# Optimization experiments

Hardware: AMD Instinct MI355X
Metric: run time of the kernel (lower is better)

The kernel has to match this reference:

```python
import jax, jax.numpy as jnp
import numpy as np

DT = 0.01   # integrator timestep (init kwarg dt)
N = 2048    # connectome.n
T = 2048    # number of timesteps
MAG_SCALE = 1e-06  # magnitude_scaling_factor applied at init


def setup_inputs() -> dict:
    key = jax.random.key(0)
    ks = jax.random.split(key, 8)
    inp = jax.random.normal(ks[0], (T, N), dtype=jnp.float32)
    sparsity_c = (jax.random.uniform(ks[1], (N, N)) < 0.1).astype(jnp.float32)
    se = (jax.random.uniform(ks[2], (N, N)) < 0.05).astype(jnp.float32)
    sparsity_e = jnp.maximum(se, se.T)
    signs_c = jnp.sign(jax.random.normal(ks[3], (N, N))).astype(jnp.float32)
    magnitudes_c = MAG_SCALE * jax.random.uniform(ks[4], (N, N), dtype=jnp.float32)
    magnitudes_e = MAG_SCALE * jax.random.uniform(ks[5], (N, N), dtype=jnp.float32)
    bias = jax.random.uniform(ks[6], (N,), dtype=jnp.float32, minval=0.01, maxval=0.02)
    tau = jax.random.uniform(ks[7], (N,), dtype=jnp.float32, minval=DT, maxval=0.2)
    hidden_init = jnp.zeros((N,), dtype=jnp.float32)
    return {
        'input': inp,
        'sparsity_c': sparsity_c,
        'sparsity_e': sparsity_e,
        'signs_c': signs_c,
        'magnitudes_c': magnitudes_c,
        'magnitudes_e': magnitudes_e,
        'bias': bias,
        'tau': tau,
        'hidden_init': hidden_init,
    }


def reference(input, sparsity_c, sparsity_e, signs_c, magnitudes_c, magnitudes_e, bias, tau, hidden_init):
    # clamp magnitudes at 0 (torch does in-place clamp_ on .data; inputs are
    # nonnegative so this is an identity with matching gradients)
    mc = jnp.maximum(magnitudes_c, 0.0)
    me = jnp.maximum(magnitudes_e, 0.0)
    W_c = sparsity_c * mc * signs_c                 # [N, N] chemical weights
    W_e = sparsity_e * (me + me.T)                  # [N, N] symmetric gap junctions
    we_row = jnp.sum(W_e, axis=1)                   # [N] row sums for diffusion term
    tau_c = jnp.maximum(tau, DT)
    alpha = DT / tau_c                              # [N]

    def step(x, u_t):
        # x: [N] hidden state, u_t: [N] external input at time t
        chem = W_c @ jax.nn.relu(x)                 # sparse chemical input
        # elec[i] = sum_j W_e[i,j] * (x[j] - x[i])  (gap-junction diffusion)
        elec = W_e @ x - we_row * x
        rec = chem + elec
        x_new = alpha * (rec + bias + u_t - x) + x
        return x_new, (x_new, rec)

    _, (hidden_states, recurrent_in) = jax.lax.scan(step, hidden_init, input)
    external_in = input  # cat of input[t].unsqueeze(0) over t == input itself
    return hidden_states, recurrent_in, external_in
```

## Files before the change

kernel.cpp:

```cpp
#include <hip/hip_runtime.h>
#include <hip/hip_bf16.h>

typedef unsigned short u16;
typedef __attribute__((ext_vector_type(8))) short bf16x8;
typedef __attribute__((ext_vector_type(4))) float f32x4;

#define N_ 2048
#define T_ 2048
#define K_ 4096
#define DT_ 0.01f
#define C_ 64
#define L_ 32

#define AS1 __attribute__((address_space(1)))
#define AS3 __attribute__((address_space(3)))
#define GLDS(gp, lp) __builtin_amdgcn_global_load_lds((const AS1 void*)(gp), (AS3 void*)(lp), 16, 0, 0)

__device__ __forceinline__ float waveReduceSum(float v){
#pragma unroll
  for (int o = 32; o > 0; o >>= 1) v += __shfl_down(v, o, 64);
  return v;
}

__global__ __launch_bounds__(256) void k1_build_zero_scan1A(
    const float* __restrict__ sc, const float* __restrict__ mc, const float* __restrict__ sg,
    __hip_bfloat16* __restrict__ Bt, float* __restrict__ we_row,
    const float* __restrict__ u, const float* __restrict__ bias, const float* __restrict__ tau,
    float* __restrict__ S1){
  int b = blockIdx.x, t = threadIdx.x;
  if (b < 2048){
    size_t g = ((size_t)b * 256 + t) * 8;
    float4 s0 = *(const float4*)(sc + g), s1 = *(const float4*)(sc + g + 4);
    float4 m0 = *(const float4*)(mc + g), m1 = *(const float4*)(mc + g + 4);
    float4 g0 = *(const float4*)(sg + g), g1 = *(const float4*)(sg + g + 4);
    __align__(16) __hip_bfloat16 o[8];
    o[0] = __float2bfloat16(s0.x * fmaxf(m0.x, 0.f) * g0.x);
    o[1] = __float2bfloat16(s0.y * fmaxf(m0.y, 0.f) * g0.y);
    o[2] = __float2bfloat16(s0.z * fmaxf(m0.z, 0.f) * g0.z);
    o[3] = __float2bfloat16(s0.w * fmaxf(m0.w, 0.f) * g0.w);
    o[4] = __float2bfloat16(s1.x * fmaxf(m1.x, 0.f) * g1.x);
    o[5] = __float2bfloat16(s1.y * fmaxf(m1.y, 0.f) * g1.y);
    o[6] = __float2bfloat16(s1.z * fmaxf(m1.z, 0.f) * g1.z);
    o[7] = __float2bfloat16(s1.w * fmaxf(m1.w, 0.f) * g1.w);
    int n = (int)(g >> 11);
    int kk = (int)(g & 2047);
    *(uint4*)&Bt[(size_t)n * K_ + kk] = *(const uint4*)o;
  } else if (b < 2056){
    we_row[(b - 2048) * 256 + t] = 0.f;
  } else {
    int bb = b - 2056;
    int c = bb >> 3;
    int i = (bb & 7) * 256 + t;
    float a  = DT_ / fmaxf(tau[i], DT_);
    float m  = 1.f - a;
    float bv = bias[i];
    float s  = 0.f;
    const float* up = u + (size_t)(c * L_) * N_ + i;
#pragma unroll 8
    for (int j = 0; j < L_; ++j)
      s = __builtin_fmaf(m, s, a * (bv + up[(size_t)j * N_]));
    S1[(size_t)c * N_ + i] = s;
  }
}

__global__ __launch_bounds__(256) void k2_prep_scan1B(
    const float* __restrict__ se, const float* __restrict__ me,
    __hip_bfloat16* __restrict__ Bt, float* __restrict__ we_row,
    const float* __restrict__ tau, const float* __restrict__ h0,
    const float* __restrict__ S1, float* __restrict__ X1){
  __shared__ float L0[64 * 65];
  __shared__ float L1[64 * 65];
  int b = blockIdx.x, t = threadIdx.x;
  if (b < 528){
    int lane = t & 63, w = t >> 6;
    int bi = 0, off = 0;
    while (off + (32 - bi) <= b){ off += 32 - bi; ++bi; }
    int bj = bi + (b - off);
    int n0 = bi * 64, j0 = bj * 64;
#pragma unroll
    for (int k = 0; k < 16; ++k){
      int r = w + 4 * k;
      size_t i1 = (size_t)(n0 + r) * N_ + j0 + lane;
      L0[r * 65 + lane] = se[i1] * fmaxf(me[i1], 0.f);
      size_t i2 = (size_t)(j0 + r) * N_ + n0 + lane;
      L1[lane * 65 + r] = se[i2] * fmaxf(me[i2], 0.f);
    }
    __syncthreads();
#pragma unroll
    for (int k = 0; k < 16; ++k){
      int nr = w + 4 * k;
      float v = L0[nr * 65 + lane] + L1[nr * 65 + lane];
      Bt[(size_t)(n0 + nr) * K_ + N_ + j0 + lane] = __float2bfloat16(v);
      L0[nr * 65 + lane] = v;
      float s = waveReduceSum(v);
      if (lane == 0) atomicAdd(&we_row[n0 + nr], s);
    }
    if (bi != bj){
      __syncthreads();
#pragma unroll
      for (int k = 0; k < 16; ++k){
        int jr = w + 4 * k;
        float v = L0[lane * 65 + jr];
        Bt[(size_t)(j0 + jr) * K_ + N_ + n0 + lane] = __float2bfloat16(v);
        float s = waveReduceSum(v);
        if (lane == 0) atomicAdd(&we_row[j0 + jr], s);
      }
    }
  } else {
    int i = (b - 528) * 256 + t;
    float a = DT_ / fmaxf(tau[i], DT_);
    float m = 1.f - a;
    float mL = m * m; mL = mL * mL; mL = mL * mL; mL = mL * mL; mL = mL * mL;
    float x = h0[i];
#pragma unroll 16
    for (int c = 0; c < C_; ++c){
      X1[(size_t)c * N_ + i] = x;
      x = __builtin_fmaf(mL, x, S1[(size_t)c * N_ + i]);
    }
  }
}

__global__ __launch_bounds__(256) void scan1C(const float* __restrict__ u, const float* __restrict__ bias,
                                              const float* __restrict__ tau, const float* __restrict__ X,
                                              __hip_bfloat16* __restrict__ A){
  int b = blockIdx.x;
  int c = b >> 3;
  int i = (b & 7) * 256 + threadIdx.x;
  float a  = DT_ / fmaxf(tau[i], DT_);
  float m  = 1.f - a;
  float bb = bias[i];
  float x  = X[(size_t)c * N_ + i];
  int t0 = c * L_;
#pragma unroll 8
  for (int j = 0; j < L_; ++j){
    size_t t = (size_t)(t0 + j);
    A[t * K_ + i]      = __float2bfloat16(fmaxf(x, 0.f));
    A[t * K_ + N_ + i] = __float2bfloat16(x);
    x = __builtin_fmaf(m, x, a * (bb + u[t * N_ + i]));
  }
}

__global__ __launch_bounds__(256) void scan2A(const float* __restrict__ u, const float* __restrict__ rec,
                                              const float* __restrict__ bias, const float* __restrict__ tau,
                                              const float* __restrict__ we_row, float* __restrict__ S){
  int b = blockIdx.x;
  int c = b >> 3;
  int i = (b & 7) * 256 + threadIdx.x;
  float a  = DT_ / fmaxf(tau[i], DT_);
  float wr = we_row[i];
  float m  = 1.f - a - a * wr;
  float bb = bias[i];
  float s  = 0.f;
  size_t base = (size_t)(c * L_) * N_ + i;
#pragma unroll 8
  for (int j = 0; j < L_; ++j){
    size_t o = base + (size_t)j * N_;
    s = __builtin_fmaf(m, s, a * (rec[o] + bb + u[o]));
  }
  S[(size_t)c * N_ + i] = s;
}

__global__ __launch_bounds__(256) void scan2B(const float* __restrict__ tau, const float* __restrict__ h0,
                                              const float* __restrict__ we_row, const float* __restrict__ S,
                                              float* __restrict__ X){
  int i = blockIdx.x * 256 + threadIdx.x;
  float a  = DT_ / fmaxf(tau[i], DT_);
  float wr = we_row[i];
  float m  = 1.f - a - a * wr;
  float mL = m * m; mL = mL * mL; mL = mL * mL; mL = mL * mL; mL = mL * mL;
  float x = h0[i];
#pragma unroll 16
  for (int c = 0; c < C_; ++c){
    X[(size_t)c * N_ + i] = x;
    x = __builtin_fmaf(mL, x, S[(size_t)c * N_ + i]);
  }
}

__global__ __launch_bounds__(256) void scan2C(const float* __restrict__ u, const float* __restrict__ bias,
                                              const float* __restrict__ tau, const float* __restrict__ we_row,
                                              const float* __restrict__ X,
                                              float* __restrict__ rec, float* __restrict__ hidden,
                                              float* __restrict__ ext){
  int b = blockIdx.x;
  int c = b >> 3;
  int i = (b & 7) * 256 + threadIdx.x;
  float a  = DT_ / fmaxf(tau[i], DT_);
  float wr = we_row[i];
  float m  = 1.f - a - a * wr;
  float bb = bias[i];
  float x  = X[(size_t)c * N_ + i];
  int t0 = c * L_;
#pragma unroll 4
  for (int j = 0; j < L_; ++j){
    size_t o = (size_t)(t0 + j) * N_ + i;
    float g  = rec[o];
    float uu = u[o];
    float cc = a * (g + bb + uu);
    rec[o]   = g - wr * x;
    if (ext) ext[o] = uu;
    x = __builtin_fmaf(m, x, cc);
    hidden[o] = x;
  }
}

__global__ __launch_bounds__(256) void copy_ext(const float4* __restrict__ in, float4* __restrict__ out){
  int i = blockIdx.x * 256 + threadIdx.x;
  out[i] = in[i];
}

__global__ __launch_bounds__(512, 4) void gemm_bt(const u16* __restrict__ A, const u16* __restrict__ B,
                                                  float* __restrict__ C){
  __shared__ __align__(16) u16 As[3][128 * 64];
  __shared__ __align__(16) u16 Bs[3][64 * 64];
  int bid = blockIdx.x;
  int j8 = bid >> 3;
  int bm = ((bid & 7) * 2 + (j8 >> 5)) * 128;
  int bn = (j8 & 31) * 64;
  int t = threadIdx.x;
  int lane = t & 63;
  int wv = t >> 6;
  int wr = (wv >> 1) * 32;
  int wc = (wv & 1) * 32;

  int srow = t >> 3;
  int scol = ((t & 7) ^ (srow & 7)) * 8;
  const u16* Ap = A + (size_t)(bm + srow) * K_ + scol;
  const u16* Bp = B + (size_t)(bn + srow) * K_ + scol;
  int lb = wv * 512;

  const f32x4 z = {0.f, 0.f, 0.f, 0.f};
  f32x4 acc[2][2];
#pragma unroll
  for (int mi = 0; mi < 2; ++mi)
#pragma unroll
    for (int ni = 0; ni < 2; ++ni) acc[mi][ni] = z;

  auto stage = [&](int buf, int kt){
    int k0 = kt * 64;
    GLDS(Ap + k0, &As[buf][lb]);
    GLDS(Ap + (size_t)64 * K_ + k0, &As[buf][4096 + lb]);
    GLDS(Bp + k0, &Bs[buf][lb]);
  };

  int fr = lane & 15, q = lane >> 4;
  auto compute = [&](int cur){
#pragma unroll
    for (int ks = 0; ks < 2; ++ks){
      bf16x8 af[2], bv[2];
#pragma unroll
      for (int mi = 0; mi < 2; ++mi){
        int r = wr + mi * 16 + fr;
        af[mi] = *(const bf16x8*)&As[cur][r * 64 + ((((ks << 2) + q) ^ (r & 7)) << 3)];
      }
#pragma unroll
      for (int ni = 0; ni < 2; ++ni){
        int r = wc + ni * 16 + fr;
        bv[ni] = *(const bf16x8*)&Bs[cur][r * 64 + ((((ks << 2) + q) ^ (r & 7)) << 3)];
      }
      __builtin_amdgcn_s_setprio(1);
#pragma unroll
      for (int mi = 0; mi < 2; ++mi)
#pragma unroll
        for (int ni = 0; ni < 2; ++ni)
          acc[mi][ni] = __builtin_amdgcn_mfma_f32_16x16x32_bf16(af[mi], bv[ni], acc[mi][ni], 0, 0, 0);
      __builtin_amdgcn_s_setprio(0);
    }
  };

  stage(0, 0);
  stage(1, 1);
  int cb = 0, sb = 2;
  for (int tt = 0; tt < 62; ++tt){
    stage(sb, tt + 2);
    asm volatile("s_waitcnt vmcnt(6)\n\ts_barrier" ::: "memory");
    compute(cb);
    asm volatile("s_barrier" ::: "memory");
    cb = (cb == 2) ? 0 : cb + 1;
    sb = (sb == 2) ? 0 : sb + 1;
  }
  asm volatile("s_waitcnt vmcnt(3)\n\ts_barrier" ::: "memory");
  compute(cb);
  cb = (cb == 2) ? 0 : cb + 1;
  asm volatile("s_waitcnt vmcnt(0)\n\ts_barrier" ::: "memory");
  compute(cb);

#pragma unroll
  for (int mi = 0; mi < 2; ++mi){
#pragma unroll
    for (int ni = 0; ni < 2; ++ni){
      int col = bn + wc + ni * 16 + fr;
#pragma unroll
      for (int r = 0; r < 4; ++r){
        int row = bm + wr + mi * 16 + q * 4 + r;
        C[(size_t)row * N_ + col] = acc[mi][ni][r];
      }
    }
  }
}

extern "C" void kernel_launch(void* const* d_in, const int* in_sizes, int n_in,
                              void* d_out, int out_size, void* d_ws, size_t ws_size,
                              hipStream_t stream){
  const float* input = (const float*)d_in[0];
  const float* sp_c  = (const float*)d_in[1];
  const float* sp_e  = (const float*)d_in[2];
  const float* sg_c  = (const float*)d_in[3];
  const float* mg_c  = (const float*)d_in[4];
  const float* mg_e  = (const float*)d_in[5];
  const float* bias  = (const float*)d_in[6];
  const float* tau   = (const float*)d_in[7];
  const float* h0    = (const float*)d_in[8];

  float* hidden = (float*)d_out;
  float* rec    = hidden + (size_t)T_ * N_;
  float* ext    = rec    + (size_t)T_ * N_;
  __hip_bfloat16* Abuf = (__hip_bfloat16*)hidden;
  __hip_bfloat16* Bt   = (__hip_bfloat16*)ext;
  float* S1 = rec;
  float* X1 = rec + (size_t)N_ * C_;
  float* we_row = (float*)d_ws;

  bool ws_ok = ws_size >= (size_t)(2048 + 2 * C_ * N_) * 4;
  float* S2 = ws_ok ? (we_row + 2048) : ext;
  float* X2 = S2 + (size_t)C_ * N_;

  k1_build_zero_scan1A<<<2568, 256, 0, stream>>>(sp_c, mg_c, sg_c, Bt, we_row,
                                                 input, bias, tau, S1);
  k2_prep_scan1B<<<536, 256, 0, stream>>>(sp_e, mg_e, Bt, we_row, tau, h0, S1, X1);
  scan1C<<<8 * C_, 256, 0, stream>>>(input, bias, tau, X1, Abuf);

  gemm_bt<<<512, 512, 0, stream>>>((const u16*)Abuf, (const u16*)Bt, rec);

  scan2A<<<8 * C_, 256, 0, stream>>>(input, rec, bias, tau, we_row, S2);
  scan2B<<<8, 256, 0, stream>>>(tau, h0, we_row, S2, X2);
  scan2C<<<8 * C_, 256, 0, stream>>>(input, bias, tau, we_row, X2, rec, hidden,
                                     ws_ok ? ext : nullptr);
  if (!ws_ok)
    copy_ext<<<T_ * N_ / 1024, 256, 0, stream>>>((const float4*)input, (float4*)ext);
}
```

Baseline: 130.8 us.

## Enlarge GEMM tiles to 128x128 and split K in two with atomic accumulation

Rewrites the bf16 GEMM to use 128x128 output tiles with 256 threads, each wave computing a 64x64 sub-tile. Shared memory drops from triple to double buffering. K is split in half across blocks, and partial results are combined with atomicAdd into a buffer zeroed by a new memset. The intent is more data reuse per block and more MFMA work per wave. In exchange it adds a full-output memset and atomic read-modify-write traffic, and shortens the prefetch depth.

```diff
diff --git a/kernel.cpp b/kernel.cpp
--- a/kernel.cpp
+++ b/kernel.cpp
@@ -208,91 +208,90 @@
   out[i] = in[i];
 }
 
-__global__ __launch_bounds__(512, 4) void gemm_bt(const u16* __restrict__ A, const u16* __restrict__ B,
+__global__ __launch_bounds__(256, 2) void gemm_bt(const u16* __restrict__ A, const u16* __restrict__ B,
                                                   float* __restrict__ C){
-  __shared__ __align__(16) u16 As[3][128 * 64];
-  __shared__ __align__(16) u16 Bs[3][64 * 64];
+  __shared__ __align__(16) u16 As[2][128 * 64];
+  __shared__ __align__(16) u16 Bs[2][128 * 64];
   int bid = blockIdx.x;
-  int j8 = bid >> 3;
-  int bm = ((bid & 7) * 2 + (j8 >> 5)) * 128;
-  int bn = (j8 & 31) * 64;
+  int xcd = bid & 7;
+  int j = bid >> 3;
+  int kh = j >> 5;
+  int jj = j & 31;
+  int bm = (xcd * 2 + (jj >> 4)) * 128;
+  int bn = (jj & 15) * 128;
+  int kbase = kh * 2048;
   int t = threadIdx.x;
   int lane = t & 63;
   int wv = t >> 6;
-  int wr = (wv >> 1) * 32;
-  int wc = (wv & 1) * 32;
+  int wr = (wv >> 1) * 64;
+  int wc = (wv & 1) * 64;
 
   int srow = t >> 3;
   int scol = ((t & 7) ^ (srow & 7)) * 8;
-  const u16* Ap = A + (size_t)(bm + srow) * K_ + scol;
-  const u16* Bp = B + (size_t)(bn + srow) * K_ + scol;
+  const u16* Ap = A + (size_t)(bm + srow) * K_ + kbase + scol;
+  const u16* Bp = B + (size_t)(bn + srow) * K_ + kbase + scol;
   int lb = wv * 512;
 
   const f32x4 z = {0.f, 0.f, 0.f, 0.f};
-  f32x4 acc[2][2];
-#pragma unroll
-  for (int mi = 0; mi < 2; ++mi)
-#pragma unroll
-    for (int ni = 0; ni < 2; ++ni) acc[mi][ni] = z;
+  f32x4 acc[4][4];
+#pragma unroll
+  for (int mi = 0; mi < 4; ++mi)
+#pragma unroll
+    for (int ni = 0; ni < 4; ++ni) acc[mi][ni] = z;
 
   auto stage = [&](int buf, int kt){
     int k0 = kt * 64;
-    GLDS(Ap + k0, &As[buf][lb]);
-    GLDS(Ap + (size_t)64 * K_ + k0, &As[buf][4096 + lb]);
-    GLDS(Bp + k0, &Bs[buf][lb]);
+#pragma unroll
+    for (int i = 0; i < 4; ++i){
+      GLDS(Ap + (size_t)(i * 32) * K_ + k0, &As[buf][i * 2048 + lb]);
+      GLDS(Bp + (size_t)(i * 32) * K_ + k0, &Bs[buf][i * 2048 + lb]);
+    }
   };
 
   int fr = lane & 15, q = lane >> 4;
   auto compute = [&](int cur){
 #pragma unroll
     for (int ks = 0; ks < 2; ++ks){
-      bf16x8 af[2], bv[2];
-#pragma unroll
-      for (int mi = 0; mi < 2; ++mi){
+      bf16x8 af[4], bv[4];
+#pragma unroll
+      for (int mi = 0; mi < 4; ++mi){
         int r = wr + mi * 16 + fr;
         af[mi] = *(const bf16x8*)&As[cur][r * 64 + ((((ks << 2) + q) ^ (r & 7)) << 3)];
       }
 #pragma unroll
-      for (int ni = 0; ni < 2; ++ni){
+      for (int ni = 0; ni < 4; ++ni){
         int r = wc + ni * 16 + fr;
         bv[ni] = *(const bf16x8*)&Bs[cur][r * 64 + ((((ks << 2) + q) ^ (r & 7)) << 3)];
       }
       __builtin_amdgcn_s_setprio(1);
 #pragma unroll
-      for (int mi = 0; mi < 2; ++mi)
-#pragma unroll
-        for (int ni = 0; ni < 2; ++ni)
+      for (int mi = 0; mi < 4; ++mi)
+#pragma unroll
+        for (int ni = 0; ni < 4; ++ni)
           acc[mi][ni] = __builtin_amdgcn_mfma_f32_16x16x32_bf16(af[mi], bv[ni], acc[mi][ni], 0, 0, 0);
       __builtin_amdgcn_s_setprio(0);
     }
   };
 
   stage(0, 0);
-  stage(1, 1);
-  int cb = 0, sb = 2;
-  for (int tt = 0; tt < 62; ++tt){
-    stage(sb, tt + 2);
-    asm volatile("s_waitcnt vmcnt(6)\n\ts_barrier" ::: "memory");
-    compute(cb);
+  for (int tt = 0; tt < 31; ++tt){
+    stage((tt + 1) & 1, tt + 1);
+    asm volatile("s_waitcnt vmcnt(8)\n\ts_barrier" ::: "memory");
+    compute(tt & 1);
     asm volatile("s_barrier" ::: "memory");
-    cb = (cb == 2) ? 0 : cb + 1;
-    sb = (sb == 2) ? 0 : sb + 1;
-  }
-  asm volatile("s_waitcnt vmcnt(3)\n\ts_barrier" ::: "memory");
-  compute(cb);
-  cb = (cb == 2) ? 0 : cb + 1;
+  }
   asm volatile("s_waitcnt vmcnt(0)\n\ts_barrier" ::: "memory");
-  compute(cb);
-
-#pragma unroll
-  for (int mi = 0; mi < 2; ++mi){
-#pragma unroll
-    for (int ni = 0; ni < 2; ++ni){
+  compute(1);
+
+#pragma unroll
+  for (int mi = 0; mi < 4; ++mi){
+#pragma unroll
+    for (int ni = 0; ni < 4; ++ni){
       int col = bn + wc + ni * 16 + fr;
 #pragma unroll
       for (int r = 0; r < 4; ++r){
         int row = bm + wr + mi * 16 + q * 4 + r;
-        C[(size_t)row * N_ + col] = acc[mi][ni][r];
+        atomicAdd(&C[(size_t)row * N_ + col], acc[mi][ni][r]);
       }
     }
   }
@@ -329,7 +328,8 @@
   k2_prep_scan1B<<<536, 256, 0, stream>>>(sp_e, mg_e, Bt, we_row, tau, h0, S1, X1);
   scan1C<<<8 * C_, 256, 0, stream>>>(input, bias, tau, X1, Abuf);
 
-  gemm_bt<<<512, 512, 0, stream>>>((const u16*)Abuf, (const u16*)Bt, rec);
+  hipMemsetAsync(rec, 0, (size_t)T_ * N_ * sizeof(float), stream);
+  gemm_bt<<<512, 256, 0, stream>>>((const u16*)Abuf, (const u16*)Bt, rec);
 
   scan2A<<<8 * C_, 256, 0, stream>>>(input, rec, bias, tau, we_row, S2);
   scan2B<<<8, 256, 0, stream>>>(tau, h0, we_row, S2, X2);
```

Measured after the change: 142.4 us. 8.8% more time.

## Fuse chunk-sum scan into GEMM epilogue and drop scan2A pass

Applied to the files above, without the earlier changes.

The per-chunk affine scan sum S2 is split into two parts. The input-driven part is computed inside scan1C. The recurrent part is folded into the GEMM epilogue, which weights each accumulator row by a power of the decay factor, reduces across lanes, and adds the result into S2. This removes the scan2A kernel, which reread the full rec and input arrays. The GEMM also drops from triple to double buffering of LDS tiles, which may raise occupancy but reduces latency hiding. The epilogue uses a non-atomic += from two column-halves (wr groups) that map to distinct cg values, so it relies on each (cg, col) being written by exactly one wave.

```diff
diff --git a/kernel.cpp b/kernel.cpp
--- a/kernel.cpp
+++ b/kernel.cpp
@@ -121,23 +121,29 @@
 }
 
 __global__ __launch_bounds__(256) void scan1C(const float* __restrict__ u, const float* __restrict__ bias,
-                                              const float* __restrict__ tau, const float* __restrict__ X,
-                                              __hip_bfloat16* __restrict__ A){
+                                              const float* __restrict__ tau, const float* __restrict__ we_row,
+                                              const float* __restrict__ X,
+                                              __hip_bfloat16* __restrict__ A, float* __restrict__ S2u){
   int b = blockIdx.x;
   int c = b >> 3;
   int i = (b & 7) * 256 + threadIdx.x;
   float a  = DT_ / fmaxf(tau[i], DT_);
   float m  = 1.f - a;
+  float m2 = 1.f - a - a * we_row[i];
   float bb = bias[i];
   float x  = X[(size_t)c * N_ + i];
+  float s2 = 0.f;
   int t0 = c * L_;
 #pragma unroll 8
   for (int j = 0; j < L_; ++j){
     size_t t = (size_t)(t0 + j);
     A[t * K_ + i]      = __float2bfloat16(fmaxf(x, 0.f));
     A[t * K_ + N_ + i] = __float2bfloat16(x);
-    x = __builtin_fmaf(m, x, a * (bb + u[t * N_ + i]));
-  }
+    float au = a * (bb + u[t * N_ + i]);
+    s2 = __builtin_fmaf(m2, s2, au);
+    x  = __builtin_fmaf(m,  x,  au);
+  }
+  if (S2u) S2u[(size_t)c * N_ + i] = s2;
 }
 
 __global__ __launch_bounds__(256) void scan2A(const float* __restrict__ u, const float* __restrict__ rec,
@@ -147,8 +153,7 @@
   int c = b >> 3;
   int i = (b & 7) * 256 + threadIdx.x;
   float a  = DT_ / fmaxf(tau[i], DT_);
-  float wr = we_row[i];
-  float m  = 1.f - a - a * wr;
+  float m  = 1.f - a - a * we_row[i];
   float bb = bias[i];
   float s  = 0.f;
   size_t base = (size_t)(c * L_) * N_ + i;
@@ -165,8 +170,7 @@
                                               float* __restrict__ X){
   int i = blockIdx.x * 256 + threadIdx.x;
   float a  = DT_ / fmaxf(tau[i], DT_);
-  float wr = we_row[i];
-  float m  = 1.f - a - a * wr;
+  float m  = 1.f - a - a * we_row[i];
   float mL = m * m; mL = mL * mL; mL = mL * mL; mL = mL * mL; mL = mL * mL;
   float x = h0[i];
 #pragma unroll 16
@@ -209,9 +213,12 @@
 }
 
 __global__ __launch_bounds__(512, 4) void gemm_bt(const u16* __restrict__ A, const u16* __restrict__ B,
-                                                  float* __restrict__ C){
-  __shared__ __align__(16) u16 As[3][128 * 64];
-  __shared__ __align__(16) u16 Bs[3][64 * 64];
+                                                  float* __restrict__ C,
+                                                  const float* __restrict__ tau,
+                                                  const float* __restrict__ we_row,
+                                                  float* __restrict__ Sbuf){
+  __shared__ __align__(16) u16 As[2][128 * 64];
+  __shared__ __align__(16) u16 Bs[2][64 * 64];
   int bid = blockIdx.x;
   int j8 = bid >> 3;
   int bm = ((bid & 7) * 2 + (j8 >> 5)) * 128;
@@ -235,8 +242,7 @@
 #pragma unroll
     for (int ni = 0; ni < 2; ++ni) acc[mi][ni] = z;
 
-  auto stage = [&](int buf, int kt){
-    int k0 = kt * 64;
+  auto stage = [&](int buf, int k0){
     GLDS(Ap + k0, &As[buf][lb]);
     GLDS(Ap + (size_t)64 * K_ + k0, &As[buf][4096 + lb]);
     GLDS(Bp + k0, &Bs[buf][lb]);
@@ -268,21 +274,14 @@
   };
 
   stage(0, 0);
-  stage(1, 1);
-  int cb = 0, sb = 2;
-  for (int tt = 0; tt < 62; ++tt){
-    stage(sb, tt + 2);
-    asm volatile("s_waitcnt vmcnt(6)\n\ts_barrier" ::: "memory");
-    compute(cb);
+  for (int tt = 0; tt < 63; ++tt){
+    stage((tt + 1) & 1, (tt + 1) * 64);
+    asm volatile("s_waitcnt vmcnt(3)\n\ts_barrier" ::: "memory");
+    compute(tt & 1);
     asm volatile("s_barrier" ::: "memory");
-    cb = (cb == 2) ? 0 : cb + 1;
-    sb = (sb == 2) ? 0 : sb + 1;
-  }
-  asm volatile("s_waitcnt vmcnt(3)\n\ts_barrier" ::: "memory");
-  compute(cb);
-  cb = (cb == 2) ? 0 : cb + 1;
+  }
   asm volatile("s_waitcnt vmcnt(0)\n\ts_barrier" ::: "memory");
-  compute(cb);
+  compute(1);
 
 #pragma unroll
   for (int mi = 0; mi < 2; ++mi){
@@ -294,6 +293,30 @@
         int row = bm + wr + mi * 16 + q * 4 + r;
         C[(size_t)row * N_ + col] = acc[mi][ni][r];
       }
+    }
+  }
+
+  if (Sbuf){
+    int cg = (bm + wr) >> 5;
+    int n3 = 3 - q;
+#pragma unroll
+    for (int ni = 0; ni < 2; ++ni){
+      int col = bn + wc + ni * 16 + fr;
+      float ac = DT_ / fmaxf(tau[col], DT_);
+      float mm = 1.f - ac - ac * we_row[col];
+      float p2 = mm * mm, p4 = p2 * p2, p8 = p4 * p4, p16 = p8 * p8;
+      float s = 1.f;
+      if (n3 & 1) s *= p4;
+      if (n3 & 2) s *= p8;
+      float v0 = __builtin_fmaf(p16, acc[0][ni][0], acc[1][ni][0]);
+      float v1 = __builtin_fmaf(p16, acc[0][ni][1], acc[1][ni][1]);
+      float v2 = __builtin_fmaf(p16, acc[0][ni][2], acc[1][ni][2]);
+      float v3 = __builtin_fmaf(p16, acc[0][ni][3], acc[1][ni][3]);
+      float part = ac * s * (v0 * (p2 * mm) + v1 * p2 + v2 * mm + v3);
+      part += __shfl_down(part, 16, 64);
+      part += __shfl_down(part, 32, 64);
+      if (q == 0)
+        Sbuf[(size_t)cg * N_ + col] += part;
     }
   }
 }
@@ -323,18 +346,22 @@
   bool ws_ok = ws_size >= (size_t)(2048 + 2 * C_ * N_) * 4;
   float* S2 = ws_ok ? (we_row + 2048) : ext;
   float* X2 = S2 + (size_t)C_ * N_;
+  float* extArg = ws_ok ? ext : nullptr;
 
   k1_build_zero_scan1A<<<2568, 256, 0, stream>>>(sp_c, mg_c, sg_c, Bt, we_row,
                                                  input, bias, tau, S1);
   k2_prep_scan1B<<<536, 256, 0, stream>>>(sp_e, mg_e, Bt, we_row, tau, h0, S1, X1);
-  scan1C<<<8 * C_, 256, 0, stream>>>(input, bias, tau, X1, Abuf);
-
-  gemm_bt<<<512, 512, 0, stream>>>((const u16*)Abuf, (const u16*)Bt, rec);
-
-  scan2A<<<8 * C_, 256, 0, stream>>>(input, rec, bias, tau, we_row, S2);
+  scan1C<<<8 * C_, 256, 0, stream>>>(input, bias, tau, we_row, X1, Abuf,
+                                     ws_ok ? S2 : nullptr);
+
+  gemm_bt<<<512, 512, 0, stream>>>((const u16*)Abuf, (const u16*)Bt, rec,
+                                   tau, we_row, ws_ok ? S2 : nullptr);
+
+  if (!ws_ok)
+    scan2A<<<8 * C_, 256, 0, stream>>>(input, rec, bias, tau, we_row, S2);
   scan2B<<<8, 256, 0, stream>>>(tau, h0, we_row, S2, X2);
-  scan2C<<<8 * C_, 256, 0, stream>>>(input, bias, tau, we_row, X2, rec, hidden,
-                                     ws_ok ? ext : nullptr);
+  scan2C<<<8 * C_, 256, 0, stream>>>(input, bias, tau, we_row, X2, rec, hidden, extArg);
+
   if (!ws_ok)
     copy_ext<<<T_ * N_ / 1024, 256, 0, stream>>>((const float4*)input, (float4*)ext);
 }
```

New measurement: 124.9 us. 1.05x faster.
